# Kernel tuning notes

Hardware: AMD Instinct MI355X
Metric: run time of the kernel (lower is better)

## Reference

```python
import jax, jax.numpy as jnp
import numpy as np

B, S, D, H = 8, 2048, 512, 8
NEG = -1e9


def setup_inputs() -> dict:
    key = jax.random.key(0)
    ks = jax.random.split(key, 12)
    inp = {
        "v": jax.random.normal(ks[0], (B, S, D), jnp.float32),
        "k": jax.random.normal(ks[1], (B, S, D), jnp.float32),
        "q": jax.random.normal(ks[2], (B, S, D), jnp.float32),
    }
    # pad_mask: 1.0 where key position is padding ([B,1,1,S]); random valid lengths
    lens = jax.random.randint(ks[3], (B,), S // 2, S + 1)
    inp["pad_mask"] = (jnp.arange(S)[None, :] >= lens[:, None]).astype(jnp.float32)[:, None, None, :]
    # head_mask: causal look-ahead mask, 1.0 above diagonal ([1,1,S,S])
    inp["head_mask"] = jnp.triu(jnp.ones((S, S), jnp.float32), k=1)[None, None]
    # Dense layer params (Keras Dense: y = x @ W + b)
    sc = 1.0 / np.sqrt(D)
    inp["Wq"] = jax.random.normal(ks[4], (D, D), jnp.float32) * sc
    inp["bq"] = jnp.zeros((D,), jnp.float32)
    inp["Wk"] = jax.random.normal(ks[5], (D, D), jnp.float32) * sc
    inp["bk"] = jnp.zeros((D,), jnp.float32)
    inp["Wv"] = jax.random.normal(ks[6], (D, D), jnp.float32) * sc
    inp["bv"] = jnp.zeros((D,), jnp.float32)
    inp["Wo"] = jax.random.normal(ks[7], (D, D), jnp.float32) * sc
    inp["bo"] = jnp.zeros((D,), jnp.float32)
    inp["num_heads"] = H
    return inp


def reference(v, k, q, pad_mask, head_mask, Wq, bq, Wk, bk, Wv, bv, Wo, bo, num_heads):
    b, s, d = q.shape
    depth = d // num_heads

    def split_heads(x):  # [b,s,d] -> [b,h,s,depth]
        return x.reshape(b, -1, num_heads, depth).transpose(0, 2, 1, 3)

    qh = split_heads(q @ Wq + bq)
    kh = split_heads(k @ Wk + bk)
    vh = split_heads(v @ Wv + bv)

    scale = 1.0 / jnp.sqrt(jnp.asarray(depth, qh.dtype))
    scores = jnp.einsum("bhqd,bhkd->bhqk", qh, kh) * scale
    scores = scores + pad_mask * NEG + head_mask * NEG
    attn = jax.nn.softmax(scores, axis=-1)
    ctx = jnp.einsum("bhqk,bhkd->bhqd", attn, vh)
    concat = ctx.transpose(0, 2, 1, 3).reshape(b, -1, d)
    return concat @ Wo + bo
```

## Files before the change

kernel.cpp:

```cpp
#include <hip/hip_runtime.h>

#define B_ 8
#define S_ 2048
#define D_ 512
#define H_ 8
#define HD_ 64

typedef __attribute__((ext_vector_type(8))) short short8;
typedef __attribute__((ext_vector_type(4))) short short4v;
typedef __attribute__((ext_vector_type(4))) float f32x4;
typedef __attribute__((ext_vector_type(16))) float f32x16;
typedef __attribute__((ext_vector_type(8))) __bf16 bf16x8;
typedef __attribute__((ext_vector_type(4))) unsigned uint4v;

__device__ __forceinline__ short f2bf(float f) {
    union { float f; unsigned u; } x; x.f = f;
    unsigned r = x.u + 0x7fffu + ((x.u >> 16) & 1u);
    return (short)(r >> 16);
}

__device__ __forceinline__ unsigned cvtpk(float a, float b) {
    unsigned r;
    asm("v_cvt_pk_bf16_f32 %0, %1, %2" : "=v"(r) : "v"(a), "v"(b));
    return r;
}

__device__ __forceinline__ f32x4 mfma16(short8 a, short8 b, f32x4 c) {
    return __builtin_amdgcn_mfma_f32_16x16x32_bf16(
        __builtin_bit_cast(bf16x8, a), __builtin_bit_cast(bf16x8, b), c, 0, 0, 0);
}

__device__ __forceinline__ f32x16 mfma32(short8 a, short8 b, f32x16 c) {
    return __builtin_amdgcn_mfma_f32_32x32x16_bf16(
        __builtin_bit_cast(bf16x8, a), __builtin_bit_cast(bf16x8, b), c, 0, 0, 0);
}

__device__ __forceinline__ f32x16 zero16() {
    f32x16 z;
    #pragma unroll
    for (int i = 0; i < 16; ++i) z[i] = 0.f;
    return z;
}

__global__ __launch_bounds__(256) void prep_wt(
    const float* __restrict__ W0, const float* __restrict__ W1,
    const float* __restrict__ W2, const float* __restrict__ W3,
    short* __restrict__ T0, short* __restrict__ T1,
    short* __restrict__ T2, short* __restrict__ T3)
{
    const float* W = (blockIdx.z == 0) ? W0 : (blockIdx.z == 1) ? W1 : (blockIdx.z == 2) ? W2 : W3;
    short* T = (blockIdx.z == 0) ? T0 : (blockIdx.z == 1) ? T1 : (blockIdx.z == 2) ? T2 : T3;
    __shared__ float t_s[64][65];
    const int tid = threadIdx.x;
    const int k0 = blockIdx.x * 64, n0 = blockIdx.y * 64;
    const int col = tid & 63, rg = tid >> 6;
    #pragma unroll
    for (int j = 0; j < 16; ++j) {
        const int row = rg * 16 + j;
        t_s[row][col] = W[(size_t)(k0 + row) * D_ + n0 + col];
    }
    __syncthreads();
    #pragma unroll
    for (int j = 0; j < 16; ++j) {
        const int nn = rg * 16 + j;
        T[(size_t)(n0 + nn) * D_ + k0 + col] = f2bf(t_s[col][nn]);
    }
}

__global__ __launch_bounds__(512) void qkv_gemm(
    const float* __restrict__ q_in, const float* __restrict__ k_in, const float* __restrict__ v_in,
    const short* __restrict__ wtq, const short* __restrict__ wtk, const short* __restrict__ wtv,
    const float* __restrict__ bq, const float* __restrict__ bk, const float* __restrict__ bv,
    short* __restrict__ qh, short* __restrict__ kh, short* __restrict__ vtb, float qscale)
{
    const int id = blockIdx.x;
    const int xcd = id & 7;
    const int slot = id >> 3;
    const int n0 = (slot & 3) * 128;
    const int pidx = xcd * 48 + (slot >> 2);
    const int z = pidx >> 7;
    const int m0 = (pidx & 127) * 128;

    const float* Ain = (z == 0) ? q_in : (z == 1) ? k_in : v_in;
    const short* Wt  = (z == 0) ? wtq  : (z == 1) ? wtk  : wtv;
    const float* bias = (z == 0) ? bq : (z == 1) ? bk : bv;
    short* Cout = (z == 0) ? qh : (z == 1) ? kh : vtb;
    const float osc = (z == 0) ? qscale : 1.0f;
    const int N = D_, K = D_;

    __shared__ __align__(16) short a_s[128 * 40];
    __shared__ __align__(16) short bt_s[128 * 40];

    const int tid = threadIdx.x;
    const int lane = tid & 63, wave = tid >> 6;
    const int wr = wave >> 2, wc = wave & 3;
    const int lr = lane & 15, lg = lane >> 4;

    const int arow = tid >> 2, ach = (tid & 3) * 8;

    f32x4 acc[4][2] = {};

    short8 avs, bvs;
    {
        const f32x4* apv = (const f32x4*)(Ain + (size_t)(m0 + arow) * K + ach);
        f32x4 f0 = apv[0], f1 = apv[1];
        const uint4v u0 = { cvtpk(f0[0], f0[1]), cvtpk(f0[2], f0[3]),
                            cvtpk(f1[0], f1[1]), cvtpk(f1[2], f1[3]) };
        avs = __builtin_bit_cast(short8, u0);
        bvs = *(const short8*)(Wt + (size_t)(n0 + arow) * K + ach);
    }

    for (int k0 = 0; k0 < K; k0 += 32) {
        __syncthreads();
        *(short8*)&a_s[arow * 40 + ach] = avs;
        *(short8*)&bt_s[arow * 40 + ach] = bvs;
        if (k0 + 32 < K) {
            const f32x4* apv = (const f32x4*)(Ain + (size_t)(m0 + arow) * K + k0 + 32 + ach);
            f32x4 f0 = apv[0], f1 = apv[1];
            const uint4v u0 = { cvtpk(f0[0], f0[1]), cvtpk(f0[2], f0[3]),
                                cvtpk(f1[0], f1[1]), cvtpk(f1[2], f1[3]) };
            avs = __builtin_bit_cast(short8, u0);
            bvs = *(const short8*)(Wt + (size_t)(n0 + arow) * K + k0 + 32 + ach);
        }
        __syncthreads();

        short8 af[4], bf[2];
        #pragma unroll
        for (int m = 0; m < 4; ++m)
            af[m] = *(const short8*)&a_s[(wr * 64 + m * 16 + lr) * 40 + lg * 8];
        #pragma unroll
        for (int n = 0; n < 2; ++n)
            bf[n] = *(const short8*)&bt_s[(wc * 32 + n * 16 + lr) * 40 + lg * 8];
        __builtin_amdgcn_s_setprio(1);
        #pragma unroll
        for (int m = 0; m < 4; ++m)
            #pragma unroll
            for (int n = 0; n < 2; ++n)
                acc[m][n] = mfma16(af[m], bf[n], acc[m][n]);
        __builtin_amdgcn_s_setprio(0);
    }

    float bvv[2];
    #pragma unroll
    for (int n = 0; n < 2; ++n) bvv[n] = bias[n0 + wc * 32 + n * 16 + lr];

    if (z == 2) {
        #pragma unroll
        for (int m = 0; m < 4; ++m) {
            const int row0 = m0 + wr * 64 + m * 16 + lg * 4;
            const int bb = row0 >> 11, s0 = row0 & (S_ - 1);
            #pragma unroll
            for (int n = 0; n < 2; ++n) {
                const int col = n0 + wc * 32 + n * 16 + lr;
                uint2 wv;
                wv.x = cvtpk(acc[m][n][0] + bvv[n], acc[m][n][1] + bvv[n]);
                wv.y = cvtpk(acc[m][n][2] + bvv[n], acc[m][n][3] + bvv[n]);
                *(uint2*)(Cout + ((size_t)col * B_ + bb) * S_ + s0) = wv;
            }
        }
    } else {
        #pragma unroll
        for (int m = 0; m < 4; ++m)
            #pragma unroll
            for (int i = 0; i < 4; ++i) {
                const size_t row = m0 + wr * 64 + m * 16 + lg * 4 + i;
                #pragma unroll
                for (int n = 0; n < 2; ++n) {
                    const int col = n0 + wc * 32 + n * 16 + lr;
                    Cout[row * N + col] = f2bf((acc[m][n][i] + bvv[n]) * osc);
                }
            }
    }
}

__global__ __launch_bounds__(512) void out_gemm(
    const short* __restrict__ Ain, const short* __restrict__ Wt,
    const float* __restrict__ bias, float* __restrict__ Cout)
{
    const int id = blockIdx.x;
    const int xcd = id & 7;
    const int slot = id >> 3;
    const int n0 = (slot & 3) * 128;
    const int m0 = (xcd * 16 + (slot >> 2)) * 128;
    const int N = D_, K = D_;

    __shared__ __align__(16) short a_s[128 * 40];
    __shared__ __align__(16) short bt_s[128 * 40];

    const int tid = threadIdx.x;
    const int lane = tid & 63, wave = tid >> 6;
    const int wr = wave >> 2, wc = wave & 3;
    const int lr = lane & 15, lg = lane >> 4;
    const int arow = tid >> 2, ach = (tid & 3) * 8;

    f32x4 acc[4][2] = {};

    short8 avs, bvs;
    {
        avs = *(const short8*)(Ain + (size_t)(m0 + arow) * K + ach);
        bvs = *(const short8*)(Wt + (size_t)(n0 + arow) * K + ach);
    }

    for (int k0 = 0; k0 < K; k0 += 32) {
        __syncthreads();
        *(short8*)&a_s[arow * 40 + ach] = avs;
        *(short8*)&bt_s[arow * 40 + ach] = bvs;
        if (k0 + 32 < K) {
            avs = *(const short8*)(Ain + (size_t)(m0 + arow) * K + k0 + 32 + ach);
            bvs = *(const short8*)(Wt + (size_t)(n0 + arow) * K + k0 + 32 + ach);
        }
        __syncthreads();

        short8 af[4], bf[2];
        #pragma unroll
        for (int m = 0; m < 4; ++m)
            af[m] = *(const short8*)&a_s[(wr * 64 + m * 16 + lr) * 40 + lg * 8];
        #pragma unroll
        for (int n = 0; n < 2; ++n)
            bf[n] = *(const short8*)&bt_s[(wc * 32 + n * 16 + lr) * 40 + lg * 8];
        __builtin_amdgcn_s_setprio(1);
        #pragma unroll
        for (int m = 0; m < 4; ++m)
            #pragma unroll
            for (int n = 0; n < 2; ++n)
                acc[m][n] = mfma16(af[m], bf[n], acc[m][n]);
        __builtin_amdgcn_s_setprio(0);
    }

    float bvv[2];
    #pragma unroll
    for (int n = 0; n < 2; ++n) bvv[n] = bias[n0 + wc * 32 + n * 16 + lr];
    #pragma unroll
    for (int m = 0; m < 4; ++m)
        #pragma unroll
        for (int i = 0; i < 4; ++i) {
            const size_t row = m0 + wr * 64 + m * 16 + lg * 4 + i;
            #pragma unroll
            for (int n = 0; n < 2; ++n)
                Cout[row * N + n0 + wc * 32 + n * 16 + lr] = acc[m][n][i] + bvv[n];
        }
}

__global__ __launch_bounds__(128, 3) void attn_k(
    const short* __restrict__ qh, const short* __restrict__ kh,
    const short* __restrict__ vt, const float* __restrict__ pad_mask,
    short* __restrict__ ctx)
{
    const int tid = threadIdx.x;
    const int lane = tid & 63, w = tid >> 6;
    const int l31 = lane & 31, hi = lane >> 5;
    const int id = blockIdx.x;
    const int h = id & 7;
    const int b = (id >> 3) & 7;
    const int pair = id >> 6;
    const int NT = S_ / 64;

    __shared__ __align__(16) short k_s[64 * 72];
    __shared__ __align__(16) short vt_s[64 * 68];
    __shared__ float red_s[2];

    const float* pb = pad_mask + (size_t)b * S_;
    {
        const f32x4* pv4 = (const f32x4*)pb;
        float psum = 0.f;
        #pragma unroll
        for (int j = 0; j < 4; ++j) {
            const f32x4 a = pv4[tid * 4 + j];
            psum += a[0] + a[1] + a[2] + a[3];
        }
        for (int off = 1; off < 64; off <<= 1) psum += __shfl_xor(psum, off);
        if (lane == 0) red_s[w] = psum;
    }
    __syncthreads();
    const int len = S_ - (int)(red_s[0] + red_s[1] + 0.5f);

    const int srow = tid >> 1, sc0 = (tid & 1) * 32;
    const short* kbase = kh + ((size_t)b * S_ + srow) * D_ + h * HD_ + sc0;
    const short* vbase = vt + ((size_t)(h * HD_ + srow) * B_ + b) * S_ + sc0;

    for (int half = 0; half < 2; ++half) {
        const int qt = half ? (NT - 1 - pair) : pair;
        const int q0 = qt * 64;
        const int kt_end = min(qt, (len - 1) >> 6);

        const int qrow = q0 + 2 * l31 + w;
        const short* qptr = qh + ((size_t)b * S_ + qrow) * D_ + h * HD_ + hi * 8;
        short8 qf[4];
        #pragma unroll
        for (int dd = 0; dd < 4; ++dd) qf[dd] = *(const short8*)(qptr + dd * 16);

        f32x16 accA = zero16(), accB = zero16();
        float m_r = -1e30f, l_r = 0.f;
        const int kmax = min(qrow, len - 1);

        short8 kv[4], vv[4];
        #pragma unroll
        for (int p = 0; p < 4; ++p) {
            kv[p] = ((const short8*)kbase)[p];
            vv[p] = ((const short8*)vbase)[p];
        }

        for (int kt = 0; kt <= kt_end; ++kt) {
            __syncthreads();
            #pragma unroll
            for (int p = 0; p < 4; ++p)
                *(short8*)&k_s[srow * 72 + sc0 + p * 8] = kv[p];
            #pragma unroll
            for (int p = 0; p < 4; ++p) {
                *(short4v*)&vt_s[srow * 68 + sc0 + p * 8]     = __builtin_shufflevector(vv[p], vv[p], 0, 1, 2, 3);
                *(short4v*)&vt_s[srow * 68 + sc0 + p * 8 + 4] = __builtin_shufflevector(vv[p], vv[p], 4, 5, 6, 7);
            }
            if (kt < kt_end) {
                const short* kp = kbase + (size_t)(kt + 1) * 64 * D_;
                const short* vp = vbase + (kt + 1) * 64;
                #pragma unroll
                for (int p = 0; p < 4; ++p) {
                    kv[p] = ((const short8*)kp)[p];
                    vv[p] = ((const short8*)vp)[p];
                }
            }
            __syncthreads();

            f32x16 scA = zero16(), scB = zero16();
            __builtin_amdgcn_s_setprio(1);
            #pragma unroll
            for (int dd = 0; dd < 4; ++dd) {
                const short8 kfA = *(const short8*)&k_s[l31 * 72 + dd * 16 + hi * 8];
                const short8 kfB = *(const short8*)&k_s[(32 + l31) * 72 + dd * 16 + hi * 8];
                scA = mfma32(kfA, qf[dd], scA);
                scB = mfma32(kfB, qf[dd], scB);
            }
            __builtin_amdgcn_s_setprio(0);

            const bool needmask = (kt == qt) || (kt * 64 + 63 >= len);
            if (needmask) {
                #pragma unroll
                for (int reg = 0; reg < 16; ++reg) {
                    const int koff = kt * 64 + (reg & 3) + 8 * (reg >> 2) + 4 * hi;
                    if (koff > kmax)      scA[reg] = -1e30f;
                    if (koff + 32 > kmax) scB[reg] = -1e30f;
                }
            }

            float m8[8], m4[4];
            #pragma unroll
            for (int i = 0; i < 8; ++i) m8[i] = fmaxf(fmaxf(scA[i], scA[i + 8]), fmaxf(scB[i], scB[i + 8]));
            #pragma unroll
            for (int i = 0; i < 4; ++i) m4[i] = fmaxf(m8[i], m8[i + 4]);
            float mt = fmaxf(fmaxf(m4[0], m4[1]), fmaxf(m4[2], m4[3]));
            mt = fmaxf(mt, __shfl_xor(mt, 32));
            const bool nogrow = __all(mt <= m_r);
            const float mn = nogrow ? m_r : fmaxf(m_r, mt);

            #pragma unroll
            for (int i = 0; i < 16; ++i) {
                scA[i] = __builtin_amdgcn_exp2f(scA[i] - mn);
                scB[i] = __builtin_amdgcn_exp2f(scB[i] - mn);
            }
            float s8[8], s4[4];
            #pragma unroll
            for (int i = 0; i < 8; ++i) s8[i] = (scA[i] + scA[i + 8]) + (scB[i] + scB[i + 8]);
            #pragma unroll
            for (int i = 0; i < 4; ++i) s4[i] = s8[i] + s8[i + 4];
            float rs = (s4[0] + s4[1]) + (s4[2] + s4[3]);
            rs += __shfl_xor(rs, 32);

            if (nogrow) {
                l_r += rs;
            } else {
                const float fac = __builtin_amdgcn_exp2f(m_r - mn);
                l_r = l_r * fac + rs;
                m_r = mn;
                #pragma unroll
                for (int reg = 0; reg < 16; ++reg) { accA[reg] *= fac; accB[reg] *= fac; }
            }

            unsigned pw[4][4];
            #pragma unroll
            for (int kk = 0; kk < 4; ++kk) {
                const int g = kk & 1;
                unsigned w0, w1, w2, w3;
                if (kk < 2) {
                    w0 = cvtpk(scA[8 * g + 0], scA[8 * g + 1]);
                    w1 = cvtpk(scA[8 * g + 2], scA[8 * g + 3]);
                    w2 = cvtpk(scA[8 * g + 4], scA[8 * g + 5]);
                    w3 = cvtpk(scA[8 * g + 6], scA[8 * g + 7]);
                } else {
                    w0 = cvtpk(scB[8 * g + 0], scB[8 * g + 1]);
                    w1 = cvtpk(scB[8 * g + 2], scB[8 * g + 3]);
                    w2 = cvtpk(scB[8 * g + 4], scB[8 * g + 5]);
                    w3 = cvtpk(scB[8 * g + 6], scB[8 * g + 7]);
                }
                asm("v_permlane32_swap_b32 %0, %1" : "+v"(w0), "+v"(w2));
                asm("v_permlane32_swap_b32 %0, %1" : "+v"(w1), "+v"(w3));
                pw[kk][0] = w0; pw[kk][1] = w1; pw[kk][2] = w2; pw[kk][3] = w3;
            }

            __builtin_amdgcn_s_setprio(1);
            #pragma unroll
            for (int kk = 0; kk < 4; ++kk) {
                const uint4v u = { pw[kk][0], pw[kk][1], pw[kk][2], pw[kk][3] };
                const short8 pf = __builtin_bit_cast(short8, u);
                const short4v a0 = *(const short4v*)&vt_s[l31 * 68 + kk * 16 + 8 * hi];
                const short4v a1 = *(const short4v*)&vt_s[l31 * 68 + kk * 16 + 8 * hi + 4];
                const short8 afA = __builtin_shufflevector(a0, a1, 0, 1, 2, 3, 4, 5, 6, 7);
                accA = mfma32(afA, pf, accA);
                const short4v b0 = *(const short4v*)&vt_s[(32 + l31) * 68 + kk * 16 + 8 * hi];
                const short4v b1 = *(const short4v*)&vt_s[(32 + l31) * 68 + kk * 16 + 8 * hi + 4];
                const short8 afB = __builtin_shufflevector(b0, b1, 0, 1, 2, 3, 4, 5, 6, 7);
                accB = mfma32(afB, pf, accB);
            }
            __builtin_amdgcn_s_setprio(0);
        }

        const float li = __builtin_amdgcn_rcpf(l_r);
        short* cp = ctx + ((size_t)b * S_ + qrow) * D_ + h * HD_ + 4 * hi;
        #pragma unroll
        for (int g = 0; g < 4; ++g) {
            uint2 wa;
            wa.x = cvtpk(accA[4 * g + 0] * li, accA[4 * g + 1] * li);
            wa.y = cvtpk(accA[4 * g + 2] * li, accA[4 * g + 3] * li);
            *(uint2*)(cp + 8 * g) = wa;
            uint2 wb;
            wb.x = cvtpk(accB[4 * g + 0] * li, accB[4 * g + 1] * li);
            wb.y = cvtpk(accB[4 * g + 2] * li, accB[4 * g + 3] * li);
            *(uint2*)(cp + 32 + 8 * g) = wb;
        }
    }
}

extern "C" void kernel_launch(void* const* d_in, const int* in_sizes, int n_in,
                              void* d_out, int out_size, void* d_ws, size_t ws_size,
                              hipStream_t stream)
{
    const float* v_in = (const float*)d_in[0];
    const float* k_in = (const float*)d_in[1];
    const float* q_in = (const float*)d_in[2];
    const float* pad  = (const float*)d_in[3];
    const float* Wq = (const float*)d_in[5];  const float* bq = (const float*)d_in[6];
    const float* Wk = (const float*)d_in[7];  const float* bk = (const float*)d_in[8];
    const float* Wv = (const float*)d_in[9];  const float* bv = (const float*)d_in[10];
    const float* Wo = (const float*)d_in[11]; const float* bo = (const float*)d_in[12];

    const size_t elems = (size_t)B_ * S_ * D_;
    const size_t welems = (size_t)D_ * D_;
    short* qh  = (short*)d_ws;
    short* kh  = qh + elems;
    short* vtb = kh + elems;
    short* ctx = vtb + elems;
    short* wtq = ctx + elems;
    short* wtk = wtq + welems;
    short* wtv = wtk + welems;
    short* wto = wtv + welems;

    prep_wt<<<dim3(D_ / 64, D_ / 64, 4), dim3(256), 0, stream>>>(Wq, Wk, Wv, Wo, wtq, wtk, wtv, wto);

    const float qscale = 0.125f * 1.4426950408889634f;
    qkv_gemm<<<dim3(1536), dim3(512), 0, stream>>>(
        q_in, k_in, v_in, wtq, wtk, wtv, bq, bk, bv, qh, kh, vtb, qscale);

    attn_k<<<dim3(1024), dim3(128), 0, stream>>>(qh, kh, vtb, pad, ctx);

    out_gemm<<<dim3(512), dim3(512), 0, stream>>>(ctx, wto, bo, (float*)d_out);
}
```

Baseline: 139.8 us.

## Widen GEMM K-tile to 128 and issue prefetch loads after barrier

The QKV and output projection GEMMs now stage a 128-wide K slice per iteration instead of 32, which cuts the number of barrier pairs from 16 to 4 and runs four MFMA sub-steps per staged tile. The next tile's global loads are issued after the second barrier so they overlap the MFMA work, and the attention kernel gets the same barrier move. In exchange, LDS per block grows from about 20KB to about 70KB and each thread holds more prefetch registers, which may reduce occupancy.

```diff
diff --git a/kernel.cpp b/kernel.cpp
--- a/kernel.cpp
+++ b/kernel.cpp
@@ -88,56 +88,64 @@
     const float osc = (z == 0) ? qscale : 1.0f;
     const int N = D_, K = D_;
 
-    __shared__ __align__(16) short a_s[128 * 40];
-    __shared__ __align__(16) short bt_s[128 * 40];
+    __shared__ __align__(16) short a_s[128 * 136];
+    __shared__ __align__(16) short bt_s[128 * 136];
 
     const int tid = threadIdx.x;
     const int lane = tid & 63, wave = tid >> 6;
     const int wr = wave >> 2, wc = wave & 3;
     const int lr = lane & 15, lg = lane >> 4;
-
-    const int arow = tid >> 2, ach = (tid & 3) * 8;
+    const int srow = tid >> 2, sch = (tid & 3) * 32;
 
     f32x4 acc[4][2] = {};
 
-    short8 avs, bvs;
+    f32x4 fa[8];
+    short8 bs[4];
     {
-        const f32x4* apv = (const f32x4*)(Ain + (size_t)(m0 + arow) * K + ach);
-        f32x4 f0 = apv[0], f1 = apv[1];
-        const uint4v u0 = { cvtpk(f0[0], f0[1]), cvtpk(f0[2], f0[3]),
-                            cvtpk(f1[0], f1[1]), cvtpk(f1[2], f1[3]) };
-        avs = __builtin_bit_cast(short8, u0);
-        bvs = *(const short8*)(Wt + (size_t)(n0 + arow) * K + ach);
-    }
-
-    for (int k0 = 0; k0 < K; k0 += 32) {
+        const f32x4* ap = (const f32x4*)(Ain + (size_t)(m0 + srow) * K + sch);
+        #pragma unroll
+        for (int j = 0; j < 8; ++j) fa[j] = ap[j];
+        const short8* bp = (const short8*)(Wt + (size_t)(n0 + srow) * K + sch);
+        #pragma unroll
+        for (int j = 0; j < 4; ++j) bs[j] = bp[j];
+    }
+
+    for (int k0 = 0; k0 < K; k0 += 128) {
         __syncthreads();
-        *(short8*)&a_s[arow * 40 + ach] = avs;
-        *(short8*)&bt_s[arow * 40 + ach] = bvs;
-        if (k0 + 32 < K) {
-            const f32x4* apv = (const f32x4*)(Ain + (size_t)(m0 + arow) * K + k0 + 32 + ach);
-            f32x4 f0 = apv[0], f1 = apv[1];
-            const uint4v u0 = { cvtpk(f0[0], f0[1]), cvtpk(f0[2], f0[3]),
-                                cvtpk(f1[0], f1[1]), cvtpk(f1[2], f1[3]) };
-            avs = __builtin_bit_cast(short8, u0);
-            bvs = *(const short8*)(Wt + (size_t)(n0 + arow) * K + k0 + 32 + ach);
+        #pragma unroll
+        for (int j = 0; j < 4; ++j) {
+            const uint4v u = { cvtpk(fa[2 * j][0], fa[2 * j][1]), cvtpk(fa[2 * j][2], fa[2 * j][3]),
+                               cvtpk(fa[2 * j + 1][0], fa[2 * j + 1][1]), cvtpk(fa[2 * j + 1][2], fa[2 * j + 1][3]) };
+            *(short8*)&a_s[srow * 136 + sch + j * 8] = __builtin_bit_cast(short8, u);
+            *(short8*)&bt_s[srow * 136 + sch + j * 8] = bs[j];
         }
         __syncthreads();
-
-        short8 af[4], bf[2];
-        #pragma unroll
-        for (int m = 0; m < 4; ++m)
-            af[m] = *(const short8*)&a_s[(wr * 64 + m * 16 + lr) * 40 + lg * 8];
-        #pragma unroll
-        for (int n = 0; n < 2; ++n)
-            bf[n] = *(const short8*)&bt_s[(wc * 32 + n * 16 + lr) * 40 + lg * 8];
-        __builtin_amdgcn_s_setprio(1);
-        #pragma unroll
-        for (int m = 0; m < 4; ++m)
+        if (k0 + 128 < K) {
+            const f32x4* ap = (const f32x4*)(Ain + (size_t)(m0 + srow) * K + k0 + 128 + sch);
+            #pragma unroll
+            for (int j = 0; j < 8; ++j) fa[j] = ap[j];
+            const short8* bp = (const short8*)(Wt + (size_t)(n0 + srow) * K + k0 + 128 + sch);
+            #pragma unroll
+            for (int j = 0; j < 4; ++j) bs[j] = bp[j];
+        }
+
+        #pragma unroll
+        for (int kc = 0; kc < 4; ++kc) {
+            short8 af[4], bf[2];
+            #pragma unroll
+            for (int m = 0; m < 4; ++m)
+                af[m] = *(const short8*)&a_s[(wr * 64 + m * 16 + lr) * 136 + kc * 32 + lg * 8];
             #pragma unroll
             for (int n = 0; n < 2; ++n)
-                acc[m][n] = mfma16(af[m], bf[n], acc[m][n]);
-        __builtin_amdgcn_s_setprio(0);
+                bf[n] = *(const short8*)&bt_s[(wc * 32 + n * 16 + lr) * 136 + kc * 32 + lg * 8];
+            __builtin_amdgcn_s_setprio(1);
+            #pragma unroll
+            for (int m = 0; m < 4; ++m)
+                #pragma unroll
+                for (int n = 0; n < 2; ++n)
+                    acc[m][n] = mfma16(af[m], bf[n], acc[m][n]);
+            __builtin_amdgcn_s_setprio(0);
+        }
     }
 
     float bvv[2];
@@ -184,47 +192,57 @@
     const int m0 = (xcd * 16 + (slot >> 2)) * 128;
     const int N = D_, K = D_;
 
-    __shared__ __align__(16) short a_s[128 * 40];
-    __shared__ __align__(16) short bt_s[128 * 40];
+    __shared__ __align__(16) short a_s[128 * 136];
+    __shared__ __align__(16) short bt_s[128 * 136];
 
     const int tid = threadIdx.x;
     const int lane = tid & 63, wave = tid >> 6;
     const int wr = wave >> 2, wc = wave & 3;
     const int lr = lane & 15, lg = lane >> 4;
-    const int arow = tid >> 2, ach = (tid & 3) * 8;
+    const int srow = tid >> 2, sch = (tid & 3) * 32;
 
     f32x4 acc[4][2] = {};
 
-    short8 avs, bvs;
+    short8 as[4], bs[4];
     {
-        avs = *(const short8*)(Ain + (size_t)(m0 + arow) * K + ach);
-        bvs = *(const short8*)(Wt + (size_t)(n0 + arow) * K + ach);
-    }
-
-    for (int k0 = 0; k0 < K; k0 += 32) {
+        const short8* ap = (const short8*)(Ain + (size_t)(m0 + srow) * K + sch);
+        const short8* bp = (const short8*)(Wt + (size_t)(n0 + srow) * K + sch);
+        #pragma unroll
+        for (int j = 0; j < 4; ++j) { as[j] = ap[j]; bs[j] = bp[j]; }
+    }
+
+    for (int k0 = 0; k0 < K; k0 += 128) {
         __syncthreads();
-        *(short8*)&a_s[arow * 40 + ach] = avs;
-        *(short8*)&bt_s[arow * 40 + ach] = bvs;
-        if (k0 + 32 < K) {
-            avs = *(const short8*)(Ain + (size_t)(m0 + arow) * K + k0 + 32 + ach);
-            bvs = *(const short8*)(Wt + (size_t)(n0 + arow) * K + k0 + 32 + ach);
+        #pragma unroll
+        for (int j = 0; j < 4; ++j) {
+            *(short8*)&a_s[srow * 136 + sch + j * 8] = as[j];
+            *(short8*)&bt_s[srow * 136 + sch + j * 8] = bs[j];
         }
         __syncthreads();
-
-        short8 af[4], bf[2];
-        #pragma unroll
-        for (int m = 0; m < 4; ++m)
-            af[m] = *(const short8*)&a_s[(wr * 64 + m * 16 + lr) * 40 + lg * 8];
-        #pragma unroll
-        for (int n = 0; n < 2; ++n)
-            bf[n] = *(const short8*)&bt_s[(wc * 32 + n * 16 + lr) * 40 + lg * 8];
-        __builtin_amdgcn_s_setprio(1);
-        #pragma unroll
-        for (int m = 0; m < 4; ++m)
+        if (k0 + 128 < K) {
+            const short8* ap = (const short8*)(Ain + (size_t)(m0 + srow) * K + k0 + 128 + sch);
+            const short8* bp = (const short8*)(Wt + (size_t)(n0 + srow) * K + k0 + 128 + sch);
+            #pragma unroll
+            for (int j = 0; j < 4; ++j) { as[j] = ap[j]; bs[j] = bp[j]; }
+        }
+
+        #pragma unroll
+        for (int kc = 0; kc < 4; ++kc) {
+            short8 af[4], bf[2];
+            #pragma unroll
+            for (int m = 0; m < 4; ++m)
+                af[m] = *(const short8*)&a_s[(wr * 64 + m * 16 + lr) * 136 + kc * 32 + lg * 8];
             #pragma unroll
             for (int n = 0; n < 2; ++n)
-                acc[m][n] = mfma16(af[m], bf[n], acc[m][n]);
-        __builtin_amdgcn_s_setprio(0);
+                bf[n] = *(const short8*)&bt_s[(wc * 32 + n * 16 + lr) * 136 + kc * 32 + lg * 8];
+            __builtin_amdgcn_s_setprio(1);
+            #pragma unroll
+            for (int m = 0; m < 4; ++m)
+                #pragma unroll
+                for (int n = 0; n < 2; ++n)
+                    acc[m][n] = mfma16(af[m], bf[n], acc[m][n]);
+            __builtin_amdgcn_s_setprio(0);
+        }
     }
 
     float bvv[2];
@@ -310,6 +328,7 @@
                 *(short4v*)&vt_s[srow * 68 + sc0 + p * 8]     = __builtin_shufflevector(vv[p], vv[p], 0, 1, 2, 3);
                 *(short4v*)&vt_s[srow * 68 + sc0 + p * 8 + 4] = __builtin_shufflevector(vv[p], vv[p], 4, 5, 6, 7);
             }
+            __syncthreads();
             if (kt < kt_end) {
                 const short* kp = kbase + (size_t)(kt + 1) * 64 * D_;
                 const short* vp = vbase + (kt + 1) * 64;
@@ -319,7 +338,6 @@
                     vv[p] = ((const short8*)vp)[p];
                 }
             }
-            __syncthreads();
 
             f32x16 scA = zero16(), scB = zero16();
             __builtin_amdgcn_s_setprio(1);
```

New measurement: 157.8 us. 12.9% more time.
